# Kernel optimization log

Measured on AMD Instinct MI355X. Metric: run time of the kernel, lower is better.

## Reference

```python
import jax, jax.numpy as jnp
import numpy as np

N_GROUP = 8
N_ITER = 3


def setup_inputs() -> dict:
    key = jax.random.key(0)
    k1, k2 = jax.random.split(key)
    B, H, W, C = 32, 28, 28, 512          # C = n_group * p = 8 * 64
    g, p, fo = N_GROUP, C // N_GROUP, 256  # per-group in-channels p, out filters fo
    x = jax.random.normal(k1, (B, H, W, C), dtype=jnp.float32)
    # per-group 1x1 conv blocks; he_normal-style scale over fan_in = p
    kernels = jax.random.normal(k2, (g, p, fo), dtype=jnp.float32) * np.float32(np.sqrt(2.0 / p))
    bias = jnp.zeros((fo,), dtype=jnp.float32)
    return {"x": x, "kernels": kernels, "bias": bias}


def reference(x, kernels, bias):
    # x: [B,H,W,g*p], kernels: [g,p,fo], bias: [fo]
    B, H, W, C = x.shape
    g, p, fo = kernels.shape
    # Grouped 1x1 conv == block-diagonal dense conv in the original (zero pads
    # kill all cross-group terms), expressed directly as a grouped contraction.
    xg = x.reshape(B, H, W, g, p)
    con = jnp.einsum('bhwgp,gpf->bhwgf', xg, kernels)  # [B,H,W,g,fo]
    # Dynamic routing over the group axis.
    beta = jnp.zeros((), dtype=con.dtype)
    out = None
    for i in range(N_ITER):
        alpha = jax.nn.sigmoid(beta)                         # scalar, then [B,H,W,g,1]
        v = jnp.sum(con * alpha, axis=-2, keepdims=True)     # [B,H,W,1,fo]
        if i == N_ITER - 1:
            out = v[..., 0, :] + bias                        # [B,H,W,fo]
        else:
            beta = beta + jnp.sum(con * v, axis=-1, keepdims=True)  # [B,H,W,g,1]
    return out


if __name__ == '__main__':
    inp = setup_inputs()
    y = jax.jit(reference)(**inp)
    print(y.shape, y.dtype)
```

## Files before the change

kernel.cpp:

```cpp
#include <hip/hip_runtime.h>

#define GRP   8
#define FO    256
#define CIN   512
#define PTILE 16
#define XROW  520
#define NTILE 1568

typedef __attribute__((ext_vector_type(8))) short bf16x8;
typedef __attribute__((ext_vector_type(4))) float f32x4;

__device__ __forceinline__ unsigned f2bu(float f) {
    unsigned u = __float_as_uint(f);
    return (u + 0x7FFFu + ((u >> 16) & 1u)) >> 16;
}
__device__ __forceinline__ short f2b(float f) { return (short)f2bu(f); }
__device__ __forceinline__ unsigned pk2(float a, float b) {
    return f2bu(a) | (f2bu(b) << 16);
}
__device__ __forceinline__ float ulo(unsigned u) { return __uint_as_float(u << 16); }
__device__ __forceinline__ float uhi(unsigned u) { return __uint_as_float(u & 0xffff0000u); }
__device__ __forceinline__ float sigmoidf_(float b) {
    return 1.0f / (1.0f + __expf(-b));
}

__global__ void repack_w(const float* __restrict__ wk, unsigned short* __restrict__ wpk) {
    int id = blockIdx.x * 256 + threadIdx.x;
    int j    = id & 7;
    int lane = (id >> 3) & 63;
    int kb   = (id >> 9) & 1;
    int t    = (id >> 10) & 15;
    int g    = id >> 14;
    int p = kb * 32 + (lane >> 4) * 8 + j;
    int f = t * 16 + (lane & 15);
    wpk[id] = (unsigned short)f2bu(wk[(g * 64 + p) * FO + f]);
}

__global__ __launch_bounds__(512, 2)
void dynroute_pk(const float* __restrict__ x, const unsigned short* __restrict__ wpk,
                 const float* __restrict__ bias, float* __restrict__ out) {
    __shared__ unsigned short xs[PTILE * XROW];
    __shared__ float part_s[8][PTILE][8];
    __shared__ float alpha1_s[PTILE][8];
    __shared__ float alpha2_s[PTILE][8];

    const int tid  = threadIdx.x;
    const int lane = tid & 63;
    const int wave = tid >> 6;
    const int pos  = lane & 15;
    const int lq   = lane >> 4;
    const long m0  = (long)blockIdx.x * PTILE;

    {
        const int row = tid >> 5;
        const int c0  = (tid & 31) * 16;
        const float* p = x + (m0 + row) * CIN + c0;
        const float4 u0 = *reinterpret_cast<const float4*>(p);
        const float4 u1 = *reinterpret_cast<const float4*>(p + 4);
        const float4 u2 = *reinterpret_cast<const float4*>(p + 8);
        const float4 u3 = *reinterpret_cast<const float4*>(p + 12);
        bf16x8 v0, v1;
        v0[0] = f2b(u0.x); v0[1] = f2b(u0.y); v0[2] = f2b(u0.z); v0[3] = f2b(u0.w);
        v0[4] = f2b(u1.x); v0[5] = f2b(u1.y); v0[6] = f2b(u1.z); v0[7] = f2b(u1.w);
        v1[0] = f2b(u2.x); v1[1] = f2b(u2.y); v1[2] = f2b(u2.z); v1[3] = f2b(u2.w);
        v1[4] = f2b(u3.x); v1[5] = f2b(u3.y); v1[6] = f2b(u3.z); v1[7] = f2b(u3.w);
        *reinterpret_cast<bf16x8*>(&xs[row * XROW + c0]) = v0;
        *reinterpret_cast<bf16x8*>(&xs[row * XROW + c0 + 8]) = v1;
    }
    __syncthreads();

    unsigned cl[2][GRP], ch[2][GRP];
    f32x4 S0 = {0.f, 0.f, 0.f, 0.f}, S1 = {0.f, 0.f, 0.f, 0.f};
    {
        const unsigned short* xrow = &xs[pos * XROW];
        const unsigned short* wb = wpk + wave * 2048 + lane * 8;
        #pragma unroll
        for (int g = 0; g < GRP; ++g) {
            const bf16x8 xf0 = *reinterpret_cast<const bf16x8*>(&xrow[g * 64 + lq * 8]);
            const bf16x8 xf1 = *reinterpret_cast<const bf16x8*>(&xrow[g * 64 + 32 + lq * 8]);
            #pragma unroll
            for (int tt = 0; tt < 2; ++tt) {
                const bf16x8 wf0 = *reinterpret_cast<const bf16x8*>(
                    wb + g * 16384 + tt * 1024);
                const bf16x8 wf1 = *reinterpret_cast<const bf16x8*>(
                    wb + g * 16384 + tt * 1024 + 512);
                f32x4 a = {0.f, 0.f, 0.f, 0.f};
                a = __builtin_amdgcn_mfma_f32_16x16x32_bf16(wf0, xf0, a, 0, 0, 0);
                a = __builtin_amdgcn_mfma_f32_16x16x32_bf16(wf1, xf1, a, 0, 0, 0);
                if (tt == 0) S0 += a; else S1 += a;
                cl[tt][g] = pk2(a[0], a[1]);
                ch[tt][g] = pk2(a[2], a[3]);
            }
        }
    }

    float d1[GRP];
    #pragma unroll
    for (int g = 0; g < GRP; ++g) {
        float s =      ulo(cl[0][g]) * S0[0];
        s = fmaf(uhi(cl[0][g]), S0[1], s);
        s = fmaf(ulo(ch[0][g]), S0[2], s);
        s = fmaf(uhi(ch[0][g]), S0[3], s);
        s = fmaf(ulo(cl[1][g]), S1[0], s);
        s = fmaf(uhi(cl[1][g]), S1[1], s);
        s = fmaf(ulo(ch[1][g]), S1[2], s);
        s = fmaf(uhi(ch[1][g]), S1[3], s);
        d1[g] = s;
    }
    #pragma unroll
    for (int g = 0; g < GRP; ++g) {
        d1[g] += __shfl_xor(d1[g], 16, 64);
        d1[g] += __shfl_xor(d1[g], 32, 64);
    }
    if (lq == 0) {
        float4 v0 = {d1[0], d1[1], d1[2], d1[3]};
        float4 v1 = {d1[4], d1[5], d1[6], d1[7]};
        *reinterpret_cast<float4*>(&part_s[wave][pos][0]) = v0;
        *reinterpret_cast<float4*>(&part_s[wave][pos][4]) = v1;
    }
    __syncthreads();

    float b1r = 0.f;
    if (tid < 128) {
        const int rp = tid >> 3, rg = tid & 7;
        float s = 0.f;
        #pragma unroll
        for (int w = 0; w < 8; ++w) s += part_s[w][rp][rg];
        b1r = 0.5f * s;
        alpha1_s[rp][rg] = sigmoidf_(b1r);
    }
    __syncthreads();

    float a1v[GRP];
    #pragma unroll
    for (int g = 0; g < GRP; ++g) a1v[g] = alpha1_s[pos][g];
    f32x4 sa0 = {0.f, 0.f, 0.f, 0.f}, sa1 = {0.f, 0.f, 0.f, 0.f};
    #pragma unroll
    for (int g = 0; g < GRP; ++g) {
        sa0[0] = fmaf(a1v[g], ulo(cl[0][g]), sa0[0]);
        sa0[1] = fmaf(a1v[g], uhi(cl[0][g]), sa0[1]);
        sa0[2] = fmaf(a1v[g], ulo(ch[0][g]), sa0[2]);
        sa0[3] = fmaf(a1v[g], uhi(ch[0][g]), sa0[3]);
        sa1[0] = fmaf(a1v[g], ulo(cl[1][g]), sa1[0]);
        sa1[1] = fmaf(a1v[g], uhi(cl[1][g]), sa1[1]);
        sa1[2] = fmaf(a1v[g], ulo(ch[1][g]), sa1[2]);
        sa1[3] = fmaf(a1v[g], uhi(ch[1][g]), sa1[3]);
    }
    float d2[GRP];
    #pragma unroll
    for (int g = 0; g < GRP; ++g) {
        float s =      ulo(cl[0][g]) * sa0[0];
        s = fmaf(uhi(cl[0][g]), sa0[1], s);
        s = fmaf(ulo(ch[0][g]), sa0[2], s);
        s = fmaf(uhi(ch[0][g]), sa0[3], s);
        s = fmaf(ulo(cl[1][g]), sa1[0], s);
        s = fmaf(uhi(cl[1][g]), sa1[1], s);
        s = fmaf(ulo(ch[1][g]), sa1[2], s);
        s = fmaf(uhi(ch[1][g]), sa1[3], s);
        d2[g] = s;
    }
    #pragma unroll
    for (int g = 0; g < GRP; ++g) {
        d2[g] += __shfl_xor(d2[g], 16, 64);
        d2[g] += __shfl_xor(d2[g], 32, 64);
    }
    if (lq == 0) {
        float4 v0 = {d2[0], d2[1], d2[2], d2[3]};
        float4 v1 = {d2[4], d2[5], d2[6], d2[7]};
        *reinterpret_cast<float4*>(&part_s[wave][pos][0]) = v0;
        *reinterpret_cast<float4*>(&part_s[wave][pos][4]) = v1;
    }
    __syncthreads();

    if (tid < 128) {
        const int rp = tid >> 3, rg = tid & 7;
        float s = 0.f;
        #pragma unroll
        for (int w = 0; w < 8; ++w) s += part_s[w][rp][rg];
        alpha2_s[rp][rg] = sigmoidf_(b1r + s);
    }
    __syncthreads();

    float a2v[GRP];
    #pragma unroll
    for (int g = 0; g < GRP; ++g) a2v[g] = alpha2_s[pos][g];
    const float4 bb0 = *reinterpret_cast<const float4*>(bias + (wave * 2 + 0) * 16 + lq * 4);
    const float4 bb1 = *reinterpret_cast<const float4*>(bias + (wave * 2 + 1) * 16 + lq * 4);
    f32x4 o0 = {bb0.x, bb0.y, bb0.z, bb0.w};
    f32x4 o1 = {bb1.x, bb1.y, bb1.z, bb1.w};
    #pragma unroll
    for (int g = 0; g < GRP; ++g) {
        o0[0] = fmaf(a2v[g], ulo(cl[0][g]), o0[0]);
        o0[1] = fmaf(a2v[g], uhi(cl[0][g]), o0[1]);
        o0[2] = fmaf(a2v[g], ulo(ch[0][g]), o0[2]);
        o0[3] = fmaf(a2v[g], uhi(ch[0][g]), o0[3]);
        o1[0] = fmaf(a2v[g], ulo(cl[1][g]), o1[0]);
        o1[1] = fmaf(a2v[g], uhi(cl[1][g]), o1[1]);
        o1[2] = fmaf(a2v[g], ulo(ch[1][g]), o1[2]);
        o1[3] = fmaf(a2v[g], uhi(ch[1][g]), o1[3]);
    }
    float* ob = out + (m0 + pos) * FO + lq * 4;
    *reinterpret_cast<float4*>(ob + (wave * 2 + 0) * 16) = *reinterpret_cast<float4*>(&o0);
    *reinterpret_cast<float4*>(ob + (wave * 2 + 1) * 16) = *reinterpret_cast<float4*>(&o1);
}

extern "C" void kernel_launch(void* const* d_in, const int* in_sizes, int n_in,
                              void* d_out, int out_size, void* d_ws, size_t ws_size,
                              hipStream_t stream) {
    const float* x    = (const float*)d_in[0];
    const float* wk   = (const float*)d_in[1];
    const float* bias = (const float*)d_in[2];
    float* out        = (float*)d_out;
    unsigned short* wpk = (unsigned short*)d_ws;

    hipLaunchKernelGGL(repack_w, dim3(512), dim3(256), 0, stream, wk, wpk);
    hipLaunchKernelGGL(dynroute_pk, dim3(NTILE), dim3(512), 0, stream,
                       x, wpk, bias, out);
}
```

Measured before the change: 55.24 us.

## Process 32 positions per block to reuse weight fragments across two tiles

Each block now handles 32 spatial positions instead of 16, so every loaded weight fragment feeds MFMAs for two position tiles, halving global weight traffic per output. The grid is halved and launch bounds ask for 4 blocks per CU. Per-thread register state doubles (cl/ch arrays), which under the tighter launch bound risks spills or reduced effective occupancy.

```diff
diff --git a/kernel.cpp b/kernel.cpp
--- a/kernel.cpp
+++ b/kernel.cpp
@@ -3,9 +3,9 @@
 #define GRP   8
 #define FO    256
 #define CIN   512
-#define PTILE 16
+#define PTILE 32
 #define XROW  520
-#define NTILE 1568
+#define NT32  784
 
 typedef __attribute__((ext_vector_type(8))) short bf16x8;
 typedef __attribute__((ext_vector_type(4))) float f32x4;
@@ -36,9 +36,9 @@
     wpk[id] = (unsigned short)f2bu(wk[(g * 64 + p) * FO + f]);
 }
 
-__global__ __launch_bounds__(512, 2)
-void dynroute_pk(const float* __restrict__ x, const unsigned short* __restrict__ wpk,
-                 const float* __restrict__ bias, float* __restrict__ out) {
+__global__ __launch_bounds__(512, 4)
+void dynroute_pk32(const float* __restrict__ x, const unsigned short* __restrict__ wpk,
+                   const float* __restrict__ bias, float* __restrict__ out) {
     __shared__ unsigned short xs[PTILE * XROW];
     __shared__ float part_s[8][PTILE][8];
     __shared__ float alpha1_s[PTILE][8];
@@ -52,76 +52,93 @@
     const long m0  = (long)blockIdx.x * PTILE;
 
     {
-        const int row = tid >> 5;
-        const int c0  = (tid & 31) * 16;
+        const int row = tid >> 4;
+        const int c0  = (tid & 15) * 32;
         const float* p = x + (m0 + row) * CIN + c0;
-        const float4 u0 = *reinterpret_cast<const float4*>(p);
-        const float4 u1 = *reinterpret_cast<const float4*>(p + 4);
-        const float4 u2 = *reinterpret_cast<const float4*>(p + 8);
-        const float4 u3 = *reinterpret_cast<const float4*>(p + 12);
-        bf16x8 v0, v1;
-        v0[0] = f2b(u0.x); v0[1] = f2b(u0.y); v0[2] = f2b(u0.z); v0[3] = f2b(u0.w);
-        v0[4] = f2b(u1.x); v0[5] = f2b(u1.y); v0[6] = f2b(u1.z); v0[7] = f2b(u1.w);
-        v1[0] = f2b(u2.x); v1[1] = f2b(u2.y); v1[2] = f2b(u2.z); v1[3] = f2b(u2.w);
-        v1[4] = f2b(u3.x); v1[5] = f2b(u3.y); v1[6] = f2b(u3.z); v1[7] = f2b(u3.w);
-        *reinterpret_cast<bf16x8*>(&xs[row * XROW + c0]) = v0;
-        *reinterpret_cast<bf16x8*>(&xs[row * XROW + c0 + 8]) = v1;
-    }
-    __syncthreads();
-
-    unsigned cl[2][GRP], ch[2][GRP];
-    f32x4 S0 = {0.f, 0.f, 0.f, 0.f}, S1 = {0.f, 0.f, 0.f, 0.f};
+        #pragma unroll
+        for (int k = 0; k < 4; ++k) {
+            const float4 u0 = *reinterpret_cast<const float4*>(p + k * 8);
+            const float4 u1 = *reinterpret_cast<const float4*>(p + k * 8 + 4);
+            bf16x8 v;
+            v[0] = f2b(u0.x); v[1] = f2b(u0.y); v[2] = f2b(u0.z); v[3] = f2b(u0.w);
+            v[4] = f2b(u1.x); v[5] = f2b(u1.y); v[6] = f2b(u1.z); v[7] = f2b(u1.w);
+            *reinterpret_cast<bf16x8*>(&xs[row * XROW + c0 + k * 8]) = v;
+        }
+    }
+    __syncthreads();
+
+    unsigned cl[2][2][GRP], ch[2][2][GRP];
     {
-        const unsigned short* xrow = &xs[pos * XROW];
         const unsigned short* wb = wpk + wave * 2048 + lane * 8;
         #pragma unroll
         for (int g = 0; g < GRP; ++g) {
-            const bf16x8 xf0 = *reinterpret_cast<const bf16x8*>(&xrow[g * 64 + lq * 8]);
-            const bf16x8 xf1 = *reinterpret_cast<const bf16x8*>(&xrow[g * 64 + 32 + lq * 8]);
+            const bf16x8 wf00 = *reinterpret_cast<const bf16x8*>(wb + g * 16384);
+            const bf16x8 wf01 = *reinterpret_cast<const bf16x8*>(wb + g * 16384 + 512);
+            const bf16x8 wf10 = *reinterpret_cast<const bf16x8*>(wb + g * 16384 + 1024);
+            const bf16x8 wf11 = *reinterpret_cast<const bf16x8*>(wb + g * 16384 + 1536);
             #pragma unroll
-            for (int tt = 0; tt < 2; ++tt) {
-                const bf16x8 wf0 = *reinterpret_cast<const bf16x8*>(
-                    wb + g * 16384 + tt * 1024);
-                const bf16x8 wf1 = *reinterpret_cast<const bf16x8*>(
-                    wb + g * 16384 + tt * 1024 + 512);
-                f32x4 a = {0.f, 0.f, 0.f, 0.f};
-                a = __builtin_amdgcn_mfma_f32_16x16x32_bf16(wf0, xf0, a, 0, 0, 0);
-                a = __builtin_amdgcn_mfma_f32_16x16x32_bf16(wf1, xf1, a, 0, 0, 0);
-                if (tt == 0) S0 += a; else S1 += a;
-                cl[tt][g] = pk2(a[0], a[1]);
-                ch[tt][g] = pk2(a[2], a[3]);
+            for (int pt = 0; pt < 2; ++pt) {
+                const unsigned short* xr = &xs[(pt * 16 + pos) * XROW + g * 64 + lq * 8];
+                const bf16x8 xf0 = *reinterpret_cast<const bf16x8*>(xr);
+                const bf16x8 xf1 = *reinterpret_cast<const bf16x8*>(xr + 32);
+                f32x4 a0 = {0.f, 0.f, 0.f, 0.f};
+                a0 = __builtin_amdgcn_mfma_f32_16x16x32_bf16(wf00, xf0, a0, 0, 0, 0);
+                a0 = __builtin_amdgcn_mfma_f32_16x16x32_bf16(wf01, xf1, a0, 0, 0, 0);
+                cl[pt][0][g] = pk2(a0[0], a0[1]);
+                ch[pt][0][g] = pk2(a0[2], a0[3]);
+                f32x4 a1 = {0.f, 0.f, 0.f, 0.f};
+                a1 = __builtin_amdgcn_mfma_f32_16x16x32_bf16(wf10, xf0, a1, 0, 0, 0);
+                a1 = __builtin_amdgcn_mfma_f32_16x16x32_bf16(wf11, xf1, a1, 0, 0, 0);
+                cl[pt][1][g] = pk2(a1[0], a1[1]);
+                ch[pt][1][g] = pk2(a1[2], a1[3]);
             }
         }
     }
 
-    float d1[GRP];
-    #pragma unroll
-    for (int g = 0; g < GRP; ++g) {
-        float s =      ulo(cl[0][g]) * S0[0];
-        s = fmaf(uhi(cl[0][g]), S0[1], s);
-        s = fmaf(ulo(ch[0][g]), S0[2], s);
-        s = fmaf(uhi(ch[0][g]), S0[3], s);
-        s = fmaf(ulo(cl[1][g]), S1[0], s);
-        s = fmaf(uhi(cl[1][g]), S1[1], s);
-        s = fmaf(ulo(ch[1][g]), S1[2], s);
-        s = fmaf(uhi(ch[1][g]), S1[3], s);
-        d1[g] = s;
-    }
-    #pragma unroll
-    for (int g = 0; g < GRP; ++g) {
-        d1[g] += __shfl_xor(d1[g], 16, 64);
-        d1[g] += __shfl_xor(d1[g], 32, 64);
-    }
+    float d1[2][GRP];
+    #pragma unroll
+    for (int pt = 0; pt < 2; ++pt) {
+        f32x4 S0 = {0.f, 0.f, 0.f, 0.f}, S1 = {0.f, 0.f, 0.f, 0.f};
+        #pragma unroll
+        for (int g = 0; g < GRP; ++g) {
+            S0[0] += ulo(cl[pt][0][g]); S0[1] += uhi(cl[pt][0][g]);
+            S0[2] += ulo(ch[pt][0][g]); S0[3] += uhi(ch[pt][0][g]);
+            S1[0] += ulo(cl[pt][1][g]); S1[1] += uhi(cl[pt][1][g]);
+            S1[2] += ulo(ch[pt][1][g]); S1[3] += uhi(ch[pt][1][g]);
+        }
+        #pragma unroll
+        for (int g = 0; g < GRP; ++g) {
+            float s =      ulo(cl[pt][0][g]) * S0[0];
+            s = fmaf(uhi(cl[pt][0][g]), S0[1], s);
+            s = fmaf(ulo(ch[pt][0][g]), S0[2], s);
+            s = fmaf(uhi(ch[pt][0][g]), S0[3], s);
+            s = fmaf(ulo(cl[pt][1][g]), S1[0], s);
+            s = fmaf(uhi(cl[pt][1][g]), S1[1], s);
+            s = fmaf(ulo(ch[pt][1][g]), S1[2], s);
+            s = fmaf(uhi(ch[pt][1][g]), S1[3], s);
+            d1[pt][g] = s;
+        }
+    }
+    #pragma unroll
+    for (int pt = 0; pt < 2; ++pt)
+        #pragma unroll
+        for (int g = 0; g < GRP; ++g) {
+            d1[pt][g] += __shfl_xor(d1[pt][g], 16, 64);
+            d1[pt][g] += __shfl_xor(d1[pt][g], 32, 64);
+        }
     if (lq == 0) {
-        float4 v0 = {d1[0], d1[1], d1[2], d1[3]};
-        float4 v1 = {d1[4], d1[5], d1[6], d1[7]};
-        *reinterpret_cast<float4*>(&part_s[wave][pos][0]) = v0;
-        *reinterpret_cast<float4*>(&part_s[wave][pos][4]) = v1;
+        #pragma unroll
+        for (int pt = 0; pt < 2; ++pt) {
+            float4 v0 = {d1[pt][0], d1[pt][1], d1[pt][2], d1[pt][3]};
+            float4 v1 = {d1[pt][4], d1[pt][5], d1[pt][6], d1[pt][7]};
+            *reinterpret_cast<float4*>(&part_s[wave][pt * 16 + pos][0]) = v0;
+            *reinterpret_cast<float4*>(&part_s[wave][pt * 16 + pos][4]) = v1;
+        }
     }
     __syncthreads();
 
     float b1r = 0.f;
-    if (tid < 128) {
+    if (tid < 256) {
         const int rp = tid >> 3, rg = tid & 7;
         float s = 0.f;
         #pragma unroll
@@ -131,48 +148,54 @@
     }
     __syncthreads();
 
-    float a1v[GRP];
-    #pragma unroll
-    for (int g = 0; g < GRP; ++g) a1v[g] = alpha1_s[pos][g];
-    f32x4 sa0 = {0.f, 0.f, 0.f, 0.f}, sa1 = {0.f, 0.f, 0.f, 0.f};
-    #pragma unroll
-    for (int g = 0; g < GRP; ++g) {
-        sa0[0] = fmaf(a1v[g], ulo(cl[0][g]), sa0[0]);
-        sa0[1] = fmaf(a1v[g], uhi(cl[0][g]), sa0[1]);
-        sa0[2] = fmaf(a1v[g], ulo(ch[0][g]), sa0[2]);
-        sa0[3] = fmaf(a1v[g], uhi(ch[0][g]), sa0[3]);
-        sa1[0] = fmaf(a1v[g], ulo(cl[1][g]), sa1[0]);
-        sa1[1] = fmaf(a1v[g], uhi(cl[1][g]), sa1[1]);
-        sa1[2] = fmaf(a1v[g], ulo(ch[1][g]), sa1[2]);
-        sa1[3] = fmaf(a1v[g], uhi(ch[1][g]), sa1[3]);
-    }
-    float d2[GRP];
-    #pragma unroll
-    for (int g = 0; g < GRP; ++g) {
-        float s =      ulo(cl[0][g]) * sa0[0];
-        s = fmaf(uhi(cl[0][g]), sa0[1], s);
-        s = fmaf(ulo(ch[0][g]), sa0[2], s);
-        s = fmaf(uhi(ch[0][g]), sa0[3], s);
-        s = fmaf(ulo(cl[1][g]), sa1[0], s);
-        s = fmaf(uhi(cl[1][g]), sa1[1], s);
-        s = fmaf(ulo(ch[1][g]), sa1[2], s);
-        s = fmaf(uhi(ch[1][g]), sa1[3], s);
-        d2[g] = s;
-    }
-    #pragma unroll
-    for (int g = 0; g < GRP; ++g) {
-        d2[g] += __shfl_xor(d2[g], 16, 64);
-        d2[g] += __shfl_xor(d2[g], 32, 64);
-    }
+    float d2[2][GRP];
+    #pragma unroll
+    for (int pt = 0; pt < 2; ++pt) {
+        f32x4 sa0 = {0.f, 0.f, 0.f, 0.f}, sa1 = {0.f, 0.f, 0.f, 0.f};
+        #pragma unroll
+        for (int g = 0; g < GRP; ++g) {
+            const float a = alpha1_s[pt * 16 + pos][g];
+            sa0[0] = fmaf(a, ulo(cl[pt][0][g]), sa0[0]);
+            sa0[1] = fmaf(a, uhi(cl[pt][0][g]), sa0[1]);
+            sa0[2] = fmaf(a, ulo(ch[pt][0][g]), sa0[2]);
+            sa0[3] = fmaf(a, uhi(ch[pt][0][g]), sa0[3]);
+            sa1[0] = fmaf(a, ulo(cl[pt][1][g]), sa1[0]);
+            sa1[1] = fmaf(a, uhi(cl[pt][1][g]), sa1[1]);
+            sa1[2] = fmaf(a, ulo(ch[pt][1][g]), sa1[2]);
+            sa1[3] = fmaf(a, uhi(ch[pt][1][g]), sa1[3]);
+        }
+        #pragma unroll
+        for (int g = 0; g < GRP; ++g) {
+            float s =      ulo(cl[pt][0][g]) * sa0[0];
+            s = fmaf(uhi(cl[pt][0][g]), sa0[1], s);
+            s = fmaf(ulo(ch[pt][0][g]), sa0[2], s);
+            s = fmaf(uhi(ch[pt][0][g]), sa0[3], s);
+            s = fmaf(ulo(cl[pt][1][g]), sa1[0], s);
+            s = fmaf(uhi(cl[pt][1][g]), sa1[1], s);
+            s = fmaf(ulo(ch[pt][1][g]), sa1[2], s);
+            s = fmaf(uhi(ch[pt][1][g]), sa1[3], s);
+            d2[pt][g] = s;
+        }
+    }
+    #pragma unroll
+    for (int pt = 0; pt < 2; ++pt)
+        #pragma unroll
+        for (int g = 0; g < GRP; ++g) {
+            d2[pt][g] += __shfl_xor(d2[pt][g], 16, 64);
+            d2[pt][g] += __shfl_xor(d2[pt][g], 32, 64);
+        }
     if (lq == 0) {
-        float4 v0 = {d2[0], d2[1], d2[2], d2[3]};
-        float4 v1 = {d2[4], d2[5], d2[6], d2[7]};
-        *reinterpret_cast<float4*>(&part_s[wave][pos][0]) = v0;
-        *reinterpret_cast<float4*>(&part_s[wave][pos][4]) = v1;
-    }
-    __syncthreads();
-
-    if (tid < 128) {
+        #pragma unroll
+        for (int pt = 0; pt < 2; ++pt) {
+            float4 v0 = {d2[pt][0], d2[pt][1], d2[pt][2], d2[pt][3]};
+            float4 v1 = {d2[pt][4], d2[pt][5], d2[pt][6], d2[pt][7]};
+            *reinterpret_cast<float4*>(&part_s[wave][pt * 16 + pos][0]) = v0;
+            *reinterpret_cast<float4*>(&part_s[wave][pt * 16 + pos][4]) = v1;
+        }
+    }
+    __syncthreads();
+
+    if (tid < 256) {
         const int rp = tid >> 3, rg = tid & 7;
         float s = 0.f;
         #pragma unroll
@@ -181,27 +204,28 @@
     }
     __syncthreads();
 
-    float a2v[GRP];
-    #pragma unroll
-    for (int g = 0; g < GRP; ++g) a2v[g] = alpha2_s[pos][g];
     const float4 bb0 = *reinterpret_cast<const float4*>(bias + (wave * 2 + 0) * 16 + lq * 4);
     const float4 bb1 = *reinterpret_cast<const float4*>(bias + (wave * 2 + 1) * 16 + lq * 4);
-    f32x4 o0 = {bb0.x, bb0.y, bb0.z, bb0.w};
-    f32x4 o1 = {bb1.x, bb1.y, bb1.z, bb1.w};
-    #pragma unroll
-    for (int g = 0; g < GRP; ++g) {
-        o0[0] = fmaf(a2v[g], ulo(cl[0][g]), o0[0]);
-        o0[1] = fmaf(a2v[g], uhi(cl[0][g]), o0[1]);
-        o0[2] = fmaf(a2v[g], ulo(ch[0][g]), o0[2]);
-        o0[3] = fmaf(a2v[g], uhi(ch[0][g]), o0[3]);
-        o1[0] = fmaf(a2v[g], ulo(cl[1][g]), o1[0]);
-        o1[1] = fmaf(a2v[g], uhi(cl[1][g]), o1[1]);
-        o1[2] = fmaf(a2v[g], ulo(ch[1][g]), o1[2]);
-        o1[3] = fmaf(a2v[g], uhi(ch[1][g]), o1[3]);
-    }
-    float* ob = out + (m0 + pos) * FO + lq * 4;
-    *reinterpret_cast<float4*>(ob + (wave * 2 + 0) * 16) = *reinterpret_cast<float4*>(&o0);
-    *reinterpret_cast<float4*>(ob + (wave * 2 + 1) * 16) = *reinterpret_cast<float4*>(&o1);
+    #pragma unroll
+    for (int pt = 0; pt < 2; ++pt) {
+        f32x4 o0 = {bb0.x, bb0.y, bb0.z, bb0.w};
+        f32x4 o1 = {bb1.x, bb1.y, bb1.z, bb1.w};
+        #pragma unroll
+        for (int g = 0; g < GRP; ++g) {
+            const float a = alpha2_s[pt * 16 + pos][g];
+            o0[0] = fmaf(a, ulo(cl[pt][0][g]), o0[0]);
+            o0[1] = fmaf(a, uhi(cl[pt][0][g]), o0[1]);
+            o0[2] = fmaf(a, ulo(ch[pt][0][g]), o0[2]);
+            o0[3] = fmaf(a, uhi(ch[pt][0][g]), o0[3]);
+            o1[0] = fmaf(a, ulo(cl[pt][1][g]), o1[0]);
+            o1[1] = fmaf(a, uhi(cl[pt][1][g]), o1[1]);
+            o1[2] = fmaf(a, ulo(ch[pt][1][g]), o1[2]);
+            o1[3] = fmaf(a, uhi(ch[pt][1][g]), o1[3]);
+        }
+        float* ob = out + (m0 + pt * 16 + pos) * FO + lq * 4;
+        *reinterpret_cast<float4*>(ob + (wave * 2 + 0) * 16) = *reinterpret_cast<float4*>(&o0);
+        *reinterpret_cast<float4*>(ob + (wave * 2 + 1) * 16) = *reinterpret_cast<float4*>(&o1);
+    }
 }
 
 extern "C" void kernel_launch(void* const* d_in, const int* in_sizes, int n_in,
@@ -214,6 +238,6 @@
     unsigned short* wpk = (unsigned short*)d_ws;
 
     hipLaunchKernelGGL(repack_w, dim3(512), dim3(256), 0, stream, wk, wpk);
-    hipLaunchKernelGGL(dynroute_pk, dim3(NTILE), dim3(512), 0, stream,
+    hipLaunchKernelGGL(dynroute_pk32, dim3(NT32), dim3(512), 0, stream,
                        x, wpk, bias, out);
 }
```

Result: slower. 182.8 us (+231.0%).
